# Performance work log

Measured on AMD Instinct MI355X. Metric: run time of the kernel, lower is better.

## Reference

```python
import jax, jax.numpy as jnp
import numpy as np

N, M, D = 16384, 16384, 16
MAX_NORM = 0.7  # keep points strictly inside Poincare ball

def _to_ball(v):
    # rescale so every point has norm < MAX_NORM
    n = jnp.linalg.norm(v, axis=1, keepdims=True)
    return MAX_NORM * v / (1.0 + n)

def setup_inputs() -> dict:
    key = jax.random.key(0)
    k1, k2 = jax.random.split(key)
    set1 = _to_ball(jax.random.normal(k1, (N, D), dtype=jnp.float32))
    set2 = _to_ball(jax.random.normal(k2, (M, D), dtype=jnp.float32))
    return {"set1": set1, "set2": set2}

def hypcdist(x, y, epsilon=0.0):
    # ||x_i - y_j||^2 for all pairs: [N, M]
    diff = x[:, None, :] - y[None, :, :]
    sqdist = jnp.sum(diff * diff, axis=-1)
    x_norm = jnp.sum(x * x, axis=1)[:, None]   # [N,1]
    y_norm = jnp.sum(y * y, axis=1)[None, :]   # [1,M]
    u = 1.0 + 2.0 * sqdist / ((1.0 - x_norm) * (1.0 - y_norm)) + epsilon
    v = jnp.sqrt(u * u - 1.0)
    return jnp.log(u + v)  # arcosh(u)

def reference(set1, set2):
    d2 = hypcdist(set1, set2)                 # [N, M]
    term_1 = jnp.mean(jnp.min(d2, axis=1))    # for each point in set1, nearest in set2
    term_2 = jnp.mean(jnp.min(d2, axis=0))    # for each point in set2, nearest in set1
    return term_1 + term_2                    # directed=False
```

## Files before the change

kernel.cpp:

```cpp
#include <hip/hip_runtime.h>
#include <math.h>

#define NPTS 16384
#define DIM  16
#define KH   32
#define CSPLIT 32
#define COLS_PER_BLOCK (NPTS / CSPLIT)
#define JT_TOTAL (COLS_PER_BLOCK / 16)
#define ROWS_PER_BLOCK 512
#define RBLK (NPTS / ROWS_PER_BLOCK)
#define MT 8
#define NBLOCKS (RBLK * CSPLIT)

typedef _Float16 f16x8 __attribute__((ext_vector_type(8)));
typedef float    f32x4 __attribute__((ext_vector_type(4)));

__global__ __launch_bounds__(256) void prep_kernel(const float* __restrict__ s1,
                                                   const float* __restrict__ s2,
                                                   _Float16* __restrict__ Xa,
                                                   _Float16* __restrict__ Yb,
                                                   unsigned int* __restrict__ rowfinal,
                                                   float* __restrict__ out) {
    int b = blockIdx.x, tid = threadIdx.x;
    int idx = b * 256 + tid;
    rowfinal[idx] = 0xFFFFFFFFu;
    if (idx == 0) out[0] = 0.f;

    int isX = (b < 64);
    const float* src = isX ? s1 : s2;
    _Float16* dst = isX ? Xa : Yb;
    int p = (isX ? b : b - 64) * 256 + tid;

    const float4* s4 = (const float4*)(src + (size_t)p * DIM);
    float4 A = s4[0], B = s4[1], C = s4[2], D = s4[3];
    float v[DIM] = {A.x,A.y,A.z,A.w, B.x,B.y,B.z,B.w,
                    C.x,C.y,C.z,C.w, D.x,D.y,D.z,D.w};
    float n2 = 0.f;
#pragma unroll
    for (int k = 0; k < DIM; ++k) n2 = fmaf(v[k], v[k], n2);
    float r = 1.0f / (1.0f - n2);

    __attribute__((aligned(16))) _Float16 buf[KH];
#pragma unroll
    for (int k = 0; k < DIM; ++k) buf[k] = (_Float16)(r * v[k]);
    if (isX) { buf[16] = (_Float16)(0.5f * r * n2);  buf[17] = (_Float16)r; }
    else     { buf[16] = (_Float16)(-r);             buf[17] = (_Float16)(-0.5f * r * n2); }
#pragma unroll
    for (int k = 18; k < KH; ++k) buf[k] = (_Float16)0.f;

    int g = p >> 4, c = p & 15;
    const uint4* b4 = (const uint4*)buf;
#pragma unroll
    for (int q = 0; q < 4; ++q) {
        size_t off = (size_t)g * 512 + (size_t)q * 128 + (size_t)c * 8;
        *(uint4*)(dst + off) = b4[q];
    }
}

__global__ __launch_bounds__(256, 2) void pairs_kernel(const _Float16* __restrict__ Xa,
                                                       const _Float16* __restrict__ Yb,
                                                       unsigned int* __restrict__ rowfinal) {
    __shared__ __align__(16) _Float16 Bs[COLS_PER_BLOCK * KH];
    __shared__ unsigned int colWave[4][COLS_PER_BLOCK];

    const int b = blockIdx.x;
    const int r  = b >> 5;
    const int cs = b & 31;

    const int tid = threadIdx.x;
    const int lane = tid & 63, w = tid >> 6;
    const int c = lane & 15, quad = lane >> 4;

    {
        const char* gsrc = (const char*)Yb + (size_t)cs * (COLS_PER_BLOCK * KH * 2)
                         + (size_t)tid * 16;
        char* lb = (char*)Bs + (size_t)tid * 16;
#pragma unroll
        for (int e = 0; e < 8; ++e) {
            __builtin_amdgcn_global_load_lds(
                (const __attribute__((address_space(1))) unsigned int*)(gsrc + e * 4096),
                (__attribute__((address_space(3))) unsigned int*)(lb + e * 4096),
                16, 0, 0);
        }
    }

    f16x8 af[MT];
#pragma unroll
    for (int t = 0; t < MT; ++t) {
        int g = r * 32 + w * 8 + t;
        af[t] = *(const f16x8*)&Xa[(size_t)g * 512 + (size_t)lane * 8];
    }

    f32x4 rowmax[MT];
#pragma unroll
    for (int t = 0; t < MT; ++t)
        rowmax[t] = (f32x4){-INFINITY, -INFINITY, -INFINITY, -INFINITY};

    const f32x4 zero = (f32x4){0.f, 0.f, 0.f, 0.f};

    __syncthreads();

#pragma unroll 2
    for (int jt = 0; jt < JT_TOTAL; ++jt) {
        f16x8 bf = *(const f16x8*)&Bs[jt * 512 + lane * 8];
        float cm = -INFINITY;
#pragma unroll
        for (int t = 0; t < MT; ++t) {
            f32x4 acc = __builtin_amdgcn_mfma_f32_16x16x32_f16(af[t], bf, zero, 0, 0, 0);
            rowmax[t][0] = fmaxf(rowmax[t][0], acc[0]);
            rowmax[t][1] = fmaxf(rowmax[t][1], acc[1]);
            rowmax[t][2] = fmaxf(rowmax[t][2], acc[2]);
            rowmax[t][3] = fmaxf(rowmax[t][3], acc[3]);
            float cv = fmaxf(fmaxf(acc[0], acc[1]), fmaxf(acc[2], acc[3]));
            cm = fmaxf(cm, cv);
        }
        cm = fmaxf(cm, __shfl_xor(cm, 16, 64));
        cm = fmaxf(cm, __shfl_xor(cm, 32, 64));
        if (quad == 0)
            colWave[w][jt * 16 + c] = __float_as_uint(cm);
    }

#pragma unroll
    for (int t = 0; t < MT; ++t) {
#pragma unroll
        for (int e = 0; e < 4; ++e) {
            float m = rowmax[t][e];
            m = fmaxf(m, __shfl_xor(m, 1, 64));
            m = fmaxf(m, __shfl_xor(m, 2, 64));
            m = fmaxf(m, __shfl_xor(m, 4, 64));
            m = fmaxf(m, __shfl_xor(m, 8, 64));
            if (c == 0) {
                int row = ((r * 32 + w * 8 + t) << 4) + quad * 4 + e;
                atomicMin(&rowfinal[row], __float_as_uint(m));
            }
        }
    }

    __syncthreads();
#pragma unroll
    for (int e = 0; e < 2; ++e) {
        int i = tid + e * 256;
        unsigned int m0 = colWave[0][i], m1 = colWave[1][i];
        unsigned int m2 = colWave[2][i], m3 = colWave[3][i];
        unsigned int m01 = m0 < m1 ? m0 : m1;
        unsigned int m23 = m2 < m3 ? m2 : m3;
        unsigned int mm  = m01 < m23 ? m01 : m23;
        atomicMin(&rowfinal[NPTS + cs * COLS_PER_BLOCK + i], mm);
    }
}

__global__ __launch_bounds__(256) void finalize_kernel(const unsigned int* __restrict__ rowfinal,
                                                       float* __restrict__ out) {
    int idx = blockIdx.x * 256 + threadIdx.x;
    float f = __uint_as_float(rowfinal[idx]);
    float t = fmaxf(-4.0f * f, 0.0f);
    float d = log1pf(t + sqrtf(t * (t + 2.0f)));
    float val = d * (1.0f / NPTS);

    __shared__ float sred[256];
    sred[threadIdx.x] = val;
    __syncthreads();
    for (int s = 128; s > 0; s >>= 1) {
        if (threadIdx.x < s) sred[threadIdx.x] += sred[threadIdx.x + s];
        __syncthreads();
    }
    if (threadIdx.x == 0) atomicAdd(out, sred[0]);
}

extern "C" void kernel_launch(void* const* d_in, const int* in_sizes, int n_in,
                              void* d_out, int out_size, void* d_ws, size_t ws_size,
                              hipStream_t stream) {
    const float* set1 = (const float*)d_in[0];
    const float* set2 = (const float*)d_in[1];
    float* out = (float*)d_out;

    _Float16* Xa = (_Float16*)d_ws;
    _Float16* Yb = Xa + (size_t)NPTS * KH;
    unsigned int* rowfinal = (unsigned int*)(Yb + (size_t)NPTS * KH);

    prep_kernel<<<128, 256, 0, stream>>>(set1, set2, Xa, Yb, rowfinal, out);
    pairs_kernel<<<NBLOCKS, 256, 0, stream>>>(Xa, Yb, rowfinal);
    finalize_kernel<<<2 * NPTS / 256, 256, 0, stream>>>(rowfinal, out);
}
```

Before: 96.67 us.

## Replace global atomicMin reductions with per-block partial buffers reduced in finalize

The pairs kernel no longer does global atomicMin on the row and column minima. Each block now writes its partial row and column maxima to dedicated slices of two partial arrays, with row results staged through shared memory so the stores are coalesced. The finalize kernel then reduces the 32 partials per point before applying arcosh. This removes atomic contention and the init pass, at the cost of about 4 MB of extra partial traffic and a longer strided read loop in finalize.

```diff
diff --git a/kernel.cpp b/kernel.cpp
--- a/kernel.cpp
+++ b/kernel.cpp
@@ -19,12 +19,9 @@
                                                    const float* __restrict__ s2,
                                                    _Float16* __restrict__ Xa,
                                                    _Float16* __restrict__ Yb,
-                                                   unsigned int* __restrict__ rowfinal,
                                                    float* __restrict__ out) {
     int b = blockIdx.x, tid = threadIdx.x;
-    int idx = b * 256 + tid;
-    rowfinal[idx] = 0xFFFFFFFFu;
-    if (idx == 0) out[0] = 0.f;
+    if (b == 0 && tid == 0) out[0] = 0.f;
 
     int isX = (b < 64);
     const float* src = isX ? s1 : s2;
@@ -59,9 +56,10 @@
 
 __global__ __launch_bounds__(256, 2) void pairs_kernel(const _Float16* __restrict__ Xa,
                                                        const _Float16* __restrict__ Yb,
-                                                       unsigned int* __restrict__ rowfinal) {
+                                                       float* __restrict__ Rpart,
+                                                       float* __restrict__ Cpart) {
     __shared__ __align__(16) _Float16 Bs[COLS_PER_BLOCK * KH];
-    __shared__ unsigned int colWave[4][COLS_PER_BLOCK];
+    __shared__ float colWave[4][COLS_PER_BLOCK];
 
     const int b = blockIdx.x;
     const int r  = b >> 5;
@@ -117,9 +115,20 @@
         cm = fmaxf(cm, __shfl_xor(cm, 16, 64));
         cm = fmaxf(cm, __shfl_xor(cm, 32, 64));
         if (quad == 0)
-            colWave[w][jt * 16 + c] = __float_as_uint(cm);
+            colWave[w][jt * 16 + c] = cm;
     }
 
+    __syncthreads();
+
+#pragma unroll
+    for (int e = 0; e < 2; ++e) {
+        int i = tid + e * 256;
+        float cm = fmaxf(fmaxf(colWave[0][i], colWave[1][i]),
+                         fmaxf(colWave[2][i], colWave[3][i]));
+        Cpart[(size_t)r * NPTS + cs * COLS_PER_BLOCK + i] = cm;
+    }
+
+    float* rowred = (float*)Bs;
 #pragma unroll
     for (int t = 0; t < MT; ++t) {
 #pragma unroll
@@ -129,31 +138,29 @@
             m = fmaxf(m, __shfl_xor(m, 2, 64));
             m = fmaxf(m, __shfl_xor(m, 4, 64));
             m = fmaxf(m, __shfl_xor(m, 8, 64));
-            if (c == 0) {
-                int row = ((r * 32 + w * 8 + t) << 4) + quad * 4 + e;
-                atomicMin(&rowfinal[row], __float_as_uint(m));
-            }
+            if (c == 0)
+                rowred[w * 128 + t * 16 + quad * 4 + e] = m;
         }
     }
-
     __syncthreads();
 #pragma unroll
     for (int e = 0; e < 2; ++e) {
         int i = tid + e * 256;
-        unsigned int m0 = colWave[0][i], m1 = colWave[1][i];
-        unsigned int m2 = colWave[2][i], m3 = colWave[3][i];
-        unsigned int m01 = m0 < m1 ? m0 : m1;
-        unsigned int m23 = m2 < m3 ? m2 : m3;
-        unsigned int mm  = m01 < m23 ? m01 : m23;
-        atomicMin(&rowfinal[NPTS + cs * COLS_PER_BLOCK + i], mm);
+        Rpart[(size_t)cs * NPTS + r * ROWS_PER_BLOCK + i] = rowred[i];
     }
 }
 
-__global__ __launch_bounds__(256) void finalize_kernel(const unsigned int* __restrict__ rowfinal,
+__global__ __launch_bounds__(256) void finalize_kernel(const float* __restrict__ Rpart,
+                                                       const float* __restrict__ Cpart,
                                                        float* __restrict__ out) {
     int idx = blockIdx.x * 256 + threadIdx.x;
-    float f = __uint_as_float(rowfinal[idx]);
-    float t = fmaxf(-4.0f * f, 0.0f);
+    const bool isRow = (idx < NPTS);
+    const float* P = isRow ? Rpart : Cpart;
+    int i = isRow ? idx : idx - NPTS;
+    float m = P[i];
+#pragma unroll 4
+    for (int s = 1; s < CSPLIT; ++s) m = fmaxf(m, P[(size_t)s * NPTS + i]);
+    float t = fmaxf(-4.0f * m, 0.0f);
     float d = log1pf(t + sqrtf(t * (t + 2.0f)));
     float val = d * (1.0f / NPTS);
 
@@ -176,9 +183,10 @@
 
     _Float16* Xa = (_Float16*)d_ws;
     _Float16* Yb = Xa + (size_t)NPTS * KH;
-    unsigned int* rowfinal = (unsigned int*)(Yb + (size_t)NPTS * KH);
+    float* Rpart = (float*)(Yb + (size_t)NPTS * KH);
+    float* Cpart = Rpart + (size_t)CSPLIT * NPTS;
 
-    prep_kernel<<<128, 256, 0, stream>>>(set1, set2, Xa, Yb, rowfinal, out);
-    pairs_kernel<<<NBLOCKS, 256, 0, stream>>>(Xa, Yb, rowfinal);
-    finalize_kernel<<<2 * NPTS / 256, 256, 0, stream>>>(rowfinal, out);
+    prep_kernel<<<128, 256, 0, stream>>>(set1, set2, Xa, Yb, out);
+    pairs_kernel<<<NBLOCKS, 256, 0, stream>>>(Xa, Yb, Rpart, Cpart);
+    finalize_kernel<<<2 * NPTS / 256, 256, 0, stream>>>(Rpart, Cpart, out);
 }
```

Result: slower. 100.9 us (+4.4%).
